# Optimization experiments

Measured on AMD Instinct MI355X. Metric: run time of the kernel, lower is better.

## Reference

```python
import jax, jax.numpy as jnp
import numpy as np

E, K, D, H = 8, 2, 1024, 2048   # num_experts, top_k, dim, ffn_dim
B, S = 1, 1024                   # batch, seq


def setup_inputs() -> dict:
    key = jax.random.key(0)
    k0, k1, k2, k3, k4 = jax.random.split(key, 5)
    sD = 1.0 / np.sqrt(D)
    sH = 1.0 / np.sqrt(H)
    return {
        "hidden_states": jax.random.normal(k0, (B, S, D), jnp.float32),
        "gate_w": jax.random.normal(k1, (E, D), jnp.float32) * sD,
        "w1": jax.random.normal(k2, (E, D, H), jnp.float32) * sD,
        "w2": jax.random.normal(k3, (E, H, D), jnp.float32) * sH,
        "w3": jax.random.normal(k4, (E, D, H), jnp.float32) * sD,
    }


def _grouped_swiglu(x_sorted, counts, w1, w2, w3):
    """Grouped expert SwiGLU over tokens sorted by expert id.

    x_sorted: [T, D] tokens grouped contiguously by expert (expert 0 first).
    counts:   [E] number of tokens per expert (sums to T).
    """
    if hasattr(jax.lax, "ragged_dot"):
        gs = counts.astype(jnp.int32)
        h = jax.nn.silu(jax.lax.ragged_dot(x_sorted, w1, gs)) * jax.lax.ragged_dot(x_sorted, w3, gs)
        return jax.lax.ragged_dot(h, w2, gs)
    # Fallback: per-expert masked GEMM (same math; zeros pass through silu*mul).
    pos = jnp.arange(x_sorted.shape[0])
    eid = jnp.searchsorted(jnp.cumsum(counts), pos, side="right")  # expert of each sorted token
    out = jnp.zeros((x_sorted.shape[0], w2.shape[-1]), x_sorted.dtype)
    for e in range(w1.shape[0]):
        xm = jnp.where((eid == e)[:, None], x_sorted, 0.0)
        he = jax.nn.silu(xm @ w1[e]) * (xm @ w3[e])
        out = out + he @ w2[e]
    return out


def reference(hidden_states, gate_w, w1, w2, w3):
    x = hidden_states.reshape(-1, D)                      # [N, D]
    N = x.shape[0]
    # --- router: softmax over experts, then top-k ---
    scores = jax.nn.softmax(x @ gate_w.T, axis=-1)        # [N, E]
    top_scores, sel = jax.lax.top_k(scores, K)            # [N, K]
    # flatten slot-major so flat_idx % N == token id (matches `% num_tokens`)
    sel_flat = sel.T.reshape(-1)                          # [K*N]
    scores_flat = top_scores.T.reshape(-1)                # [K*N]
    # --- reorder: stable sort by expert id ---
    order = jnp.argsort(sel_flat, stable=True)            # [K*N]
    tok_sorted = order % N                                # original token per routed slot
    scores_sorted = scores_flat[order]
    counts = jnp.bincount(sel_flat, length=E)             # tokens per expert
    # --- dispatch (ep_size=1: all-to-all is identity) + grouped expert GEMM ---
    x_sorted = x[tok_sorted]                              # [K*N, D]
    y = _grouped_swiglu(x_sorted, counts, w1, w2, w3)     # [K*N, D]
    # --- weighted scatter-combine ---
    weighted = y * scores_sorted[:, None]
    out = jnp.zeros((N, D), x.dtype).at[tok_sorted].add(weighted)
    return out.reshape(hidden_states.shape)
```

## Files before the change

kernel.cpp:

```cpp
#include <hip/hip_runtime.h>
#include <hip/hip_bf16.h>
#include <math.h>

#define NE 8
#define DD 1024
#define HH 2048
#define NTOK 1024
#define NSLOT 2048
#define NSLOTP 3072

typedef short short8v __attribute__((ext_vector_type(8)));
typedef short short4v __attribute__((ext_vector_type(4)));
typedef float f32x4 __attribute__((ext_vector_type(4)));

static __device__ __forceinline__ unsigned short f2bf(float f) {
  union { __hip_bfloat16 h; unsigned short u; } c;
  c.h = __float2bfloat16(f);
  return c.u;
}

static __device__ __forceinline__ int sigma(int n) {
  return ((n >> 1) & 3) ^ ((n >> 3) & 1);
}

#define GLD16(SRC, DST)                                                        \
  __builtin_amdgcn_global_load_lds(                                            \
      (__attribute__((address_space(1))) void*)(SRC),                          \
      (__attribute__((address_space(3))) void*)(DST), 16, 0, 0)

__global__ __launch_bounds__(64) void krouter(const float* __restrict__ x,
                                              const float* __restrict__ gw,
                                              int* __restrict__ e_sel,
                                              float* __restrict__ w_sel) {
  int n = blockIdx.x;
  int lane = threadIdx.x;
  const float4* xr = (const float4*)(x + (size_t)n * DD);
  const float4* gr = (const float4*)gw;
  float acc[NE];
#pragma unroll
  for (int e = 0; e < NE; ++e) acc[e] = 0.f;
#pragma unroll
  for (int i = 0; i < 4; ++i) {
    float4 xv = xr[lane + i * 64];
#pragma unroll
    for (int e = 0; e < NE; ++e) {
      float4 gv = gr[e * 256 + lane + i * 64];
      acc[e] += xv.x * gv.x + xv.y * gv.y + xv.z * gv.z + xv.w * gv.w;
    }
  }
#pragma unroll
  for (int e = 0; e < NE; ++e)
#pragma unroll
    for (int off = 32; off > 0; off >>= 1) acc[e] += __shfl_xor(acc[e], off);
  if (lane == 0) {
    float m = acc[0];
#pragma unroll
    for (int e = 1; e < NE; ++e) m = fmaxf(m, acc[e]);
    float p[NE];
    float z = 0.f;
#pragma unroll
    for (int e = 0; e < NE; ++e) { p[e] = expf(acc[e] - m); z += p[e]; }
    float inv = 1.f / z;
    int e1 = 0;
#pragma unroll
    for (int e = 1; e < NE; ++e) if (acc[e] > acc[e1]) e1 = e;
    int e2 = (e1 == 0) ? 1 : 0;
#pragma unroll
    for (int e = 0; e < NE; ++e) if (e != e1 && acc[e] > acc[e2]) e2 = e;
    e_sel[n] = e1;         w_sel[n] = p[e1] * inv;
    e_sel[NTOK + n] = e2;  w_sel[NTOK + n] = p[e2] * inv;
  }
}

__global__ __launch_bounds__(256) void kbuild(const int* __restrict__ e_sel,
                                              const float* __restrict__ w_sel,
                                              int* __restrict__ tok,
                                              float* __restrict__ wgt,
                                              int* __restrict__ meta) {
  __shared__ int sc[NE], scur[NE];
  int t = threadIdx.x;
  if (t < NE) sc[t] = 0;
  __syncthreads();
  for (int s = t; s < NSLOTP; s += 256) tok[s] = -1;
  for (int s = t; s < NSLOT; s += 256) atomicAdd(&sc[e_sel[s]], 1);
  __syncthreads();
  if (t == 0) {
    int run = 0, i64 = 0, i128 = 0;
    for (int e = 0; e < NE; ++e) {
      meta[8 + e] = run; scur[e] = run;
      meta[e] = sc[e];
      int nm = (sc[e] + 127) >> 7;
      for (int m = 0; m < nm; ++m) {
        meta[128 + i128] = e; meta[152 + i128] = m; ++i128;
      }
      for (int m = 0; m < 2 * nm; ++m) {
        meta[32 + i64] = e; meta[80 + i64] = m; ++i64;
      }
      run += nm << 7;
    }
    meta[16] = i64; meta[17] = i128;
  }
  __syncthreads();
  for (int s = t; s < NSLOT; s += 256) {
    int e = e_sel[s];
    int pos = atomicAdd(&scur[e], 1);
    tok[pos] = s & (NTOK - 1);
    wgt[pos] = w_sel[s];
  }
}

__global__ __launch_bounds__(256) void kgather(const float* __restrict__ x,
                                               const int* __restrict__ tok,
                                               unsigned short* __restrict__ xg) {
  int tid = threadIdx.x;
  int row = blockIdx.x * 2 + (tid >> 7);
  int g = tid & 127;
  int t = tok[row];
  int pos = (g & 3) ^ ((row >> 1) & 3);
  char* dst = (char*)xg + (size_t)row * 2048 + (g >> 2) * 64 + (pos << 4);
  short8v v = {0, 0, 0, 0, 0, 0, 0, 0};
  if (t >= 0) {
    const float* src = x + (size_t)t * DD + g * 8;
    float4 f0 = *(const float4*)src;
    float4 f1 = *(const float4*)(src + 4);
    v[0] = (short)f2bf(f0.x); v[1] = (short)f2bf(f0.y);
    v[2] = (short)f2bf(f0.z); v[3] = (short)f2bf(f0.w);
    v[4] = (short)f2bf(f1.x); v[5] = (short)f2bf(f1.y);
    v[6] = (short)f2bf(f1.z); v[7] = (short)f2bf(f1.w);
  }
  *(short8v*)dst = v;
}

__global__ __launch_bounds__(256, 4) void kgemm13(
    const unsigned short* __restrict__ xg, const float* __restrict__ w1,
    const float* __restrict__ w3, unsigned short* __restrict__ hws,
    const int* __restrict__ meta) {
  __shared__ __align__(16) char smem[24576];
  char* ldsA = smem;
  char* ldsB = smem + 8192;
  int vt = blockIdx.y;
  if (vt >= meta[16]) return;
  int e = meta[32 + vt], mt = meta[80 + vt];
  int n0 = blockIdx.x * 64;
  int abase = meta[8 + e] + mt * 64;
  int tid = threadIdx.x, l = tid & 63, w = tid >> 6;

  int th = tid & 127;
  int nb = th & 15, kb = th >> 4;
  const float* wsrc = (tid < 128) ? w1 : w3;
  const float* pb = wsrc + (size_t)e * DD * HH + (size_t)(kb * 4) * HH + n0 + nb * 4;
  int mofs = (tid < 128) ? 0 : 4096;
  int baddr[4];
#pragma unroll
  for (int c = 0; c < 4; ++c) {
    int n = nb * 4 + c;
    baddr[c] = mofs + n * 64 + ((((kb >> 1) ^ sigma(n)) & 3) << 4) + (kb & 1) * 8;
  }
  const char* srcA = (const char*)xg +
                     (size_t)(abase + w * 16 + (l >> 2)) * 2048 + ((l & 3) << 4);
  int aoff[4];
#pragma unroll
  for (int mf = 0; mf < 4; ++mf) {
    int r = mf * 16 + (l & 15);
    aoff[mf] = r * 64 + ((((l >> 4) ^ (r >> 1)) & 3) << 4);
  }
  int nn = w * 16 + (l & 15);
  int boff = nn * 64 + ((((l >> 4) ^ sigma(nn)) & 3) << 4);

  f32x4 accg[4], accu[4];
#pragma unroll
  for (int i = 0; i < 4; ++i) {
    accg[i] = (f32x4){0.f, 0.f, 0.f, 0.f};
    accu[i] = (f32x4){0.f, 0.f, 0.f, 0.f};
  }

  float4 q[4];
  const float* qp = pb;
#pragma unroll
  for (int r = 0; r < 4; ++r) q[r] = *(const float4*)(qp + (size_t)r * HH);
  GLD16(srcA, ldsA + w * 1024);
#pragma unroll
  for (int c = 0; c < 4; ++c) {
    short4v tv;
    tv[0] = (short)f2bf(q[0][c]); tv[1] = (short)f2bf(q[1][c]);
    tv[2] = (short)f2bf(q[2][c]); tv[3] = (short)f2bf(q[3][c]);
    *(short4v*)(ldsB + baddr[c]) = tv;
  }
  qp += 32 * HH;
#pragma unroll
  for (int r = 0; r < 4; ++r) q[r] = *(const float4*)(qp + (size_t)r * HH);
  GLD16(srcA + 64, ldsA + 4096 + w * 1024);
  qp += 32 * HH;
  __syncthreads();

  for (int s = 0; s < 32; ++s) {
    int buf = s & 1;
    short8v a[4];
#pragma unroll
    for (int mf = 0; mf < 4; ++mf)
      a[mf] = *(const short8v*)(ldsA + buf * 4096 + aoff[mf]);
    short8v bg = *(const short8v*)(ldsB + buf * 8192 + boff);
    short8v bu = *(const short8v*)(ldsB + buf * 8192 + 4096 + boff);
#pragma unroll
    for (int mf = 0; mf < 4; ++mf) {
      accg[mf] = __builtin_amdgcn_mfma_f32_16x16x32_bf16(a[mf], bg, accg[mf], 0, 0, 0);
      accu[mf] = __builtin_amdgcn_mfma_f32_16x16x32_bf16(a[mf], bu, accu[mf], 0, 0, 0);
    }
    if (s < 31) {
      char* d = ldsB + (buf ^ 1) * 8192;
#pragma unroll
      for (int c = 0; c < 4; ++c) {
        short4v tv;
        tv[0] = (short)f2bf(q[0][c]); tv[1] = (short)f2bf(q[1][c]);
        tv[2] = (short)f2bf(q[2][c]); tv[3] = (short)f2bf(q[3][c]);
        *(short4v*)(d + baddr[c]) = tv;
      }
    }
    __syncthreads();
    if (s < 30) {
#pragma unroll
      for (int r = 0; r < 4; ++r) q[r] = *(const float4*)(qp + (size_t)r * HH);
      GLD16(srcA + (s + 2) * 64, ldsA + buf * 4096 + w * 1024);
      qp += 32 * HH;
    }
  }

  unsigned short* hl = (unsigned short*)smem;
#pragma unroll
  for (int mf = 0; mf < 4; ++mf)
#pragma unroll
    for (int rr = 0; rr < 4; ++rr) {
      int row = mf * 16 + ((l >> 4) << 2) + rr;
      int col = w * 16 + (l & 15);
      float gv = accg[mf][rr], uv = accu[mf][rr];
      hl[row * 64 + col] = f2bf((gv / (1.f + __expf(-gv))) * uv);
    }
  __syncthreads();
#pragma unroll
  for (int p = 0; p < 2; ++p) {
    int idx = p * 256 + tid;
    int row = idx >> 3, g = idx & 7;
    int dp = abase + row;
    size_t db = (size_t)dp * 4096 + (size_t)n0 * 2 + (g >> 2) * 64 +
                ((size_t)((g & 3) ^ ((dp >> 1) & 3)) << 4);
    *(short8v*)((char*)hws + db) =
        *(const short8v*)((const char*)hl + row * 128 + (g << 4));
  }
}

__global__ __launch_bounds__(256, 4) void kgemm2(
    const unsigned short* __restrict__ hws, const float* __restrict__ w2,
    float* __restrict__ out, const int* __restrict__ tok,
    const float* __restrict__ wgt, const int* __restrict__ meta) {
  __shared__ __align__(16) char smem[16384];
  char* ldsA = smem;
  char* ldsB = smem + 8192;
  int vt = blockIdx.y;
  if (vt >= meta[16]) return;
  int e = meta[32 + vt], mt = meta[80 + vt];
  int n0 = blockIdx.x * 64;
  int kz = blockIdx.z;
  int mbase = meta[8 + e] + mt * 64;
  int rem = meta[e] - mt * 64;
  int tid = threadIdx.x, l = tid & 63, w = tid >> 6;

  int nb = tid & 15, kb = tid >> 4;
  const float* pb = w2 + (size_t)e * HH * DD +
                    (size_t)(kz * 1024 + kb * 2) * DD + n0 + nb * 4;
  int baddr[4];
#pragma unroll
  for (int c = 0; c < 4; ++c) {
    int n = nb * 4 + c;
    baddr[c] = n * 64 + ((((kb >> 2) ^ sigma(n)) & 3) << 4) + (kb & 3) * 4;
  }
  const char* srcA = (const char*)hws +
                     (size_t)(mbase + w * 16 + (l >> 2)) * 4096 +
                     (size_t)kz * 2048 + ((l & 3) << 4);
  int aoff[4];
#pragma unroll
  for (int mf = 0; mf < 4; ++mf) {
    int r = mf * 16 + (l & 15);
    aoff[mf] = r * 64 + ((((l >> 4) ^ (r >> 1)) & 3) << 4);
  }
  int nn = w * 16 + (l & 15);
  int boff = nn * 64 + ((((l >> 4) ^ sigma(nn)) & 3) << 4);

  f32x4 acc[4];
#pragma unroll
  for (int i = 0; i < 4; ++i) acc[i] = (f32x4){0.f, 0.f, 0.f, 0.f};

  float4 q[2];
  const float* qp = pb;
#pragma unroll
  for (int r = 0; r < 2; ++r) q[r] = *(const float4*)(qp + (size_t)r * DD);
  GLD16(srcA, ldsA + w * 1024);
  {
#pragma unroll
    for (int c = 0; c < 4; ++c) {
      unsigned v = (unsigned)f2bf(q[0][c]) | ((unsigned)f2bf(q[1][c]) << 16);
      *(unsigned*)(ldsB + baddr[c]) = v;
    }
  }
  qp += 32 * DD;
#pragma unroll
  for (int r = 0; r < 2; ++r) q[r] = *(const float4*)(qp + (size_t)r * DD);
  GLD16(srcA + 64, ldsA + 4096 + w * 1024);
  qp += 32 * DD;
  __syncthreads();

  for (int s = 0; s < 32; ++s) {
    int buf = s & 1;
    short8v a[4];
#pragma unroll
    for (int mf = 0; mf < 4; ++mf)
      a[mf] = *(const short8v*)(ldsA + buf * 4096 + aoff[mf]);
    short8v b = *(const short8v*)(ldsB + buf * 4096 + boff);
#pragma unroll
    for (int mf = 0; mf < 4; ++mf)
      acc[mf] = __builtin_amdgcn_mfma_f32_16x16x32_bf16(a[mf], b, acc[mf], 0, 0, 0);
    if (s < 31) {
      char* d = ldsB + (buf ^ 1) * 4096;
#pragma unroll
      for (int c = 0; c < 4; ++c) {
        unsigned v = (unsigned)f2bf(q[0][c]) | ((unsigned)f2bf(q[1][c]) << 16);
        *(unsigned*)(d + baddr[c]) = v;
      }
    }
    __syncthreads();
    if (s < 30) {
#pragma unroll
      for (int r = 0; r < 2; ++r) q[r] = *(const float4*)(qp + (size_t)r * DD);
      GLD16(srcA + (s + 2) * 64, ldsA + buf * 4096 + w * 1024);
      qp += 32 * DD;
    }
  }

#pragma unroll
  for (int mf = 0; mf < 4; ++mf)
#pragma unroll
    for (int rr = 0; rr < 4; ++rr) {
      int row = mf * 16 + ((l >> 4) << 2) + rr;
      if (row < rem) {
        int t = tok[mbase + row];
        float wt = wgt[mbase + row];
        atomicAdd(out + (size_t)t * DD + n0 + w * 16 + (l & 15),
                  wt * acc[mf][rr]);
      }
    }
}

extern "C" void kernel_launch(void* const* d_in, const int* in_sizes, int n_in,
                              void* d_out, int out_size, void* d_ws, size_t ws_size,
                              hipStream_t stream) {
  const float* x  = (const float*)d_in[0];
  const float* gw = (const float*)d_in[1];
  const float* w1 = (const float*)d_in[2];
  const float* w2 = (const float*)d_in[3];
  const float* w3 = (const float*)d_in[4];
  float* out = (float*)d_out;
  char* ws = (char*)d_ws;
  const size_t MB = 1024 * 1024;
  if (ws_size < 24 * MB) return;

  unsigned short* xg  = (unsigned short*)(ws);
  unsigned short* hws = (unsigned short*)(ws + 6 * MB);
  char* mb = ws + 20 * MB;
  int*   e_sel  = (int*)mb;
  float* w_sel  = (float*)(mb + 8192);
  int*   tok    = (int*)(mb + 16384);
  float* wgt    = (float*)(mb + 16384 + 12288);
  int*   meta   = (int*)(mb + 16384 + 24576);

  hipMemsetAsync(out, 0, (size_t)out_size * sizeof(float), stream);
  krouter<<<dim3(NTOK), 64, 0, stream>>>(x, gw, e_sel, w_sel);
  kbuild<<<1, 256, 0, stream>>>(e_sel, w_sel, tok, wgt, meta);
  kgather<<<dim3(NSLOTP / 2), 256, 0, stream>>>(x, tok, xg);
  kgemm13<<<dim3(32, 48), 256, 0, stream>>>(xg, w1, w3, hws, meta);
  kgemm2<<<dim3(16, 48, 2), 256, 0, stream>>>(hws, w2, out, tok, wgt, meta);
}
```

Before: 119.6 us.

## Use 128-row M tiles with register-staged A operand in expert GEMMs

Both expert GEMM kernels move from 64-row to 128-row M tiles over a 2x2 wave layout, so each fp32 weight tile is streamed and converted once per 128 routed tokens instead of once per 64. This targets the dominant cost, which is reading the fp32 w1/w3/w2 weights. The A operand is now loaded straight from global memory into registers rather than staged through LDS, which halves LDS use. Weight prefetch is deepened to two stages in registers. The costs are more accumulator registers (launch bound drops to 3 blocks), more padded rows for experts with few tokens, and reliance on 128-row tile metadata in meta[17], meta[128+] and meta[152+], which kbuild is assumed to already fill.

```diff
diff --git a/kernel.cpp b/kernel.cpp
--- a/kernel.cpp
+++ b/kernel.cpp
@@ -10,7 +10,6 @@
 #define NSLOTP 3072
 
 typedef short short8v __attribute__((ext_vector_type(8)));
-typedef short short4v __attribute__((ext_vector_type(4)));
 typedef float f32x4 __attribute__((ext_vector_type(4)));
 
 static __device__ __forceinline__ unsigned short f2bf(float f) {
@@ -23,10 +22,12 @@
   return ((n >> 1) & 3) ^ ((n >> 3) & 1);
 }
 
-#define GLD16(SRC, DST)                                                        \
-  __builtin_amdgcn_global_load_lds(                                            \
-      (__attribute__((address_space(1))) void*)(SRC),                          \
-      (__attribute__((address_space(3))) void*)(DST), 16, 0, 0)
+static __device__ __forceinline__ short8v pk8(const float* q) {
+  short8v v;
+#pragma unroll
+  for (int i = 0; i < 8; ++i) v[i] = (short)f2bf(q[i]);
+  return v;
+}
 
 __global__ __launch_bounds__(64) void krouter(const float* __restrict__ x,
                                               const float* __restrict__ gw,
@@ -121,123 +122,132 @@
   short8v v = {0, 0, 0, 0, 0, 0, 0, 0};
   if (t >= 0) {
     const float* src = x + (size_t)t * DD + g * 8;
-    float4 f0 = *(const float4*)src;
-    float4 f1 = *(const float4*)(src + 4);
-    v[0] = (short)f2bf(f0.x); v[1] = (short)f2bf(f0.y);
-    v[2] = (short)f2bf(f0.z); v[3] = (short)f2bf(f0.w);
-    v[4] = (short)f2bf(f1.x); v[5] = (short)f2bf(f1.y);
-    v[6] = (short)f2bf(f1.z); v[7] = (short)f2bf(f1.w);
+    float q[8];
+#pragma unroll
+    for (int i = 0; i < 8; ++i) q[i] = src[i];
+    v = pk8(q);
   }
   *(short8v*)dst = v;
 }
 
-__global__ __launch_bounds__(256, 4) void kgemm13(
+__global__ __launch_bounds__(256, 3) void kgemm13(
     const unsigned short* __restrict__ xg, const float* __restrict__ w1,
     const float* __restrict__ w3, unsigned short* __restrict__ hws,
     const int* __restrict__ meta) {
-  __shared__ __align__(16) char smem[24576];
-  char* ldsA = smem;
-  char* ldsB = smem + 8192;
+  __shared__ __align__(16) char smem[16384];
+  char* ldsB = smem;
   int vt = blockIdx.y;
-  if (vt >= meta[16]) return;
-  int e = meta[32 + vt], mt = meta[80 + vt];
+  if (vt >= meta[17]) return;
+  int e = meta[128 + vt], mt = meta[152 + vt];
   int n0 = blockIdx.x * 64;
-  int abase = meta[8 + e] + mt * 64;
+  int abase = meta[8 + e] + mt * 128;
   int tid = threadIdx.x, l = tid & 63, w = tid >> 6;
-
-  int th = tid & 127;
-  int nb = th & 15, kb = th >> 4;
-  const float* wsrc = (tid < 128) ? w1 : w3;
-  const float* pb = wsrc + (size_t)e * DD * HH + (size_t)(kb * 4) * HH + n0 + nb * 4;
-  int mofs = (tid < 128) ? 0 : 4096;
-  int baddr[4];
-#pragma unroll
-  for (int c = 0; c < 4; ++c) {
-    int n = nb * 4 + c;
-    baddr[c] = mofs + n * 64 + ((((kb >> 1) ^ sigma(n)) & 3) << 4) + (kb & 1) * 8;
-  }
-  const char* srcA = (const char*)xg +
-                     (size_t)(abase + w * 16 + (l >> 2)) * 2048 + ((l & 3) << 4);
-  int aoff[4];
+  int wm = w & 1, wn = w >> 1;
+
+  int bn = tid & 63, kb = tid >> 6;
+  const float* pb1 = w1 + (size_t)e * DD * HH + (size_t)(kb * 8) * HH + n0 + bn;
+  const float* pb3 = w3 + (size_t)e * DD * HH + (size_t)(kb * 8) * HH + n0 + bn;
+  int wb = bn * 64 + (((kb ^ sigma(bn)) & 3) << 4);
+
+  const char* pa[4];
 #pragma unroll
   for (int mf = 0; mf < 4; ++mf) {
-    int r = mf * 16 + (l & 15);
-    aoff[mf] = r * 64 + ((((l >> 4) ^ (r >> 1)) & 3) << 4);
-  }
-  int nn = w * 16 + (l & 15);
-  int boff = nn * 64 + ((((l >> 4) ^ sigma(nn)) & 3) << 4);
-
-  f32x4 accg[4], accu[4];
-#pragma unroll
-  for (int i = 0; i < 4; ++i) {
-    accg[i] = (f32x4){0.f, 0.f, 0.f, 0.f};
-    accu[i] = (f32x4){0.f, 0.f, 0.f, 0.f};
-  }
-
-  float4 q[4];
-  const float* qp = pb;
-#pragma unroll
-  for (int r = 0; r < 4; ++r) q[r] = *(const float4*)(qp + (size_t)r * HH);
-  GLD16(srcA, ldsA + w * 1024);
-#pragma unroll
-  for (int c = 0; c < 4; ++c) {
-    short4v tv;
-    tv[0] = (short)f2bf(q[0][c]); tv[1] = (short)f2bf(q[1][c]);
-    tv[2] = (short)f2bf(q[2][c]); tv[3] = (short)f2bf(q[3][c]);
-    *(short4v*)(ldsB + baddr[c]) = tv;
-  }
-  qp += 32 * HH;
-#pragma unroll
-  for (int r = 0; r < 4; ++r) q[r] = *(const float4*)(qp + (size_t)r * HH);
-  GLD16(srcA + 64, ldsA + 4096 + w * 1024);
-  qp += 32 * HH;
-  __syncthreads();
-
-  for (int s = 0; s < 32; ++s) {
-    int buf = s & 1;
-    short8v a[4];
-#pragma unroll
-    for (int mf = 0; mf < 4; ++mf)
-      a[mf] = *(const short8v*)(ldsA + buf * 4096 + aoff[mf]);
-    short8v bg = *(const short8v*)(ldsB + buf * 8192 + boff);
-    short8v bu = *(const short8v*)(ldsB + buf * 8192 + 4096 + boff);
-#pragma unroll
-    for (int mf = 0; mf < 4; ++mf) {
-      accg[mf] = __builtin_amdgcn_mfma_f32_16x16x32_bf16(a[mf], bg, accg[mf], 0, 0, 0);
-      accu[mf] = __builtin_amdgcn_mfma_f32_16x16x32_bf16(a[mf], bu, accu[mf], 0, 0, 0);
+    int r = wm * 64 + mf * 16 + (l & 15);
+    pa[mf] = (const char*)xg + (size_t)(abase + r) * 2048 +
+             ((((l >> 4) ^ (r >> 1)) & 3) << 4);
+  }
+  int boff[2];
+#pragma unroll
+  for (int nf = 0; nf < 2; ++nf) {
+    int n = wn * 32 + nf * 16 + (l & 15);
+    boff[nf] = n * 64 + ((((l >> 4) ^ sigma(n)) & 3) << 4);
+  }
+
+  f32x4 accg[4][2], accu[4][2];
+#pragma unroll
+  for (int i = 0; i < 4; ++i)
+#pragma unroll
+    for (int j = 0; j < 2; ++j) {
+      accg[i][j] = (f32x4){0.f, 0.f, 0.f, 0.f};
+      accu[i][j] = (f32x4){0.f, 0.f, 0.f, 0.f};
     }
-    if (s < 31) {
-      char* d = ldsB + (buf ^ 1) * 8192;
-#pragma unroll
-      for (int c = 0; c < 4; ++c) {
-        short4v tv;
-        tv[0] = (short)f2bf(q[0][c]); tv[1] = (short)f2bf(q[1][c]);
-        tv[2] = (short)f2bf(q[2][c]); tv[3] = (short)f2bf(q[3][c]);
-        *(short4v*)(d + baddr[c]) = tv;
+
+  float q1[2][8], q3[2][8];
+  short8v a[4];
+#pragma unroll
+  for (int r = 0; r < 8; ++r) {
+    q1[0][r] = pb1[(size_t)r * HH];
+    q3[0][r] = pb3[(size_t)r * HH];
+    q1[1][r] = pb1[(size_t)(32 + r) * HH];
+    q3[1][r] = pb3[(size_t)(32 + r) * HH];
+  }
+#pragma unroll
+  for (int mf = 0; mf < 4; ++mf) a[mf] = *(const short8v*)(pa[mf]);
+  *(short8v*)(ldsB + wb) = pk8(q1[0]);
+  *(short8v*)(ldsB + 4096 + wb) = pk8(q3[0]);
+#pragma unroll
+  for (int r = 0; r < 8; ++r) {
+    q1[0][r] = pb1[(size_t)(64 + r) * HH];
+    q3[0][r] = pb3[(size_t)(64 + r) * HH];
+  }
+  __syncthreads();
+
+#define STEP13(S, P)                                                           \
+  {                                                                            \
+    if ((S) < 31) {                                                            \
+      char* d = ldsB + (((P) ^ 1) << 13);                                      \
+      *(short8v*)(d + wb) = pk8(q1[(P) ^ 1]);                                  \
+      *(short8v*)(d + 4096 + wb) = pk8(q3[(P) ^ 1]);                           \
+    }                                                                          \
+    if ((S) < 29) {                                                            \
+      const float* s1 = pb1 + (size_t)((S) + 3) * 32 * HH;                     \
+      const float* s3 = pb3 + (size_t)((S) + 3) * 32 * HH;                     \
+      _Pragma("unroll") for (int r = 0; r < 8; ++r) {                          \
+        q1[(P) ^ 1][r] = s1[(size_t)r * HH];                                   \
+        q3[(P) ^ 1][r] = s3[(size_t)r * HH];                                   \
+      }                                                                        \
+    }                                                                          \
+    short8v b1f[2], b3f[2];                                                    \
+    _Pragma("unroll") for (int nf = 0; nf < 2; ++nf) {                         \
+      b1f[nf] = *(const short8v*)(ldsB + ((P) << 13) + boff[nf]);              \
+      b3f[nf] = *(const short8v*)(ldsB + ((P) << 13) + 4096 + boff[nf]);       \
+    }                                                                          \
+    _Pragma("unroll") for (int nf = 0; nf < 2; ++nf)                           \
+        _Pragma("unroll") for (int mf = 0; mf < 4; ++mf) {                     \
+      accg[mf][nf] = __builtin_amdgcn_mfma_f32_16x16x32_bf16(                  \
+          a[mf], b1f[nf], accg[mf][nf], 0, 0, 0);                              \
+      accu[mf][nf] = __builtin_amdgcn_mfma_f32_16x16x32_bf16(                  \
+          a[mf], b3f[nf], accu[mf][nf], 0, 0, 0);                              \
+    }                                                                          \
+    if ((S) < 31) {                                                           \
+      _Pragma("unroll") for (int mf = 0; mf < 4; ++mf)                         \
+          a[mf] = *(const short8v*)(pa[mf] + ((S) + 1) * 64);                  \
+    }                                                                          \
+    __syncthreads();                                                           \
+  }
+
+  for (int ss = 0; ss < 16; ++ss) {
+    int s0 = 2 * ss;
+    STEP13(s0, 0);
+    STEP13(s0 + 1, 1);
+  }
+#undef STEP13
+
+  unsigned short* hl = (unsigned short*)smem;
+#pragma unroll
+  for (int mf = 0; mf < 4; ++mf)
+#pragma unroll
+    for (int nf = 0; nf < 2; ++nf)
+#pragma unroll
+      for (int rr = 0; rr < 4; ++rr) {
+        int row = wm * 64 + mf * 16 + ((l >> 4) << 2) + rr;
+        int col = wn * 32 + nf * 16 + (l & 15);
+        float gv = accg[mf][nf][rr], uv = accu[mf][nf][rr];
+        hl[row * 64 + col] = f2bf((gv / (1.f + __expf(-gv))) * uv);
       }
-    }
-    __syncthreads();
-    if (s < 30) {
-#pragma unroll
-      for (int r = 0; r < 4; ++r) q[r] = *(const float4*)(qp + (size_t)r * HH);
-      GLD16(srcA + (s + 2) * 64, ldsA + buf * 4096 + w * 1024);
-      qp += 32 * HH;
-    }
-  }
-
-  unsigned short* hl = (unsigned short*)smem;
-#pragma unroll
-  for (int mf = 0; mf < 4; ++mf)
-#pragma unroll
-    for (int rr = 0; rr < 4; ++rr) {
-      int row = mf * 16 + ((l >> 4) << 2) + rr;
-      int col = w * 16 + (l & 15);
-      float gv = accg[mf][rr], uv = accu[mf][rr];
-      hl[row * 64 + col] = f2bf((gv / (1.f + __expf(-gv))) * uv);
-    }
-  __syncthreads();
-#pragma unroll
-  for (int p = 0; p < 2; ++p) {
+  __syncthreads();
+#pragma unroll
+  for (int p = 0; p < 4; ++p) {
     int idx = p * 256 + tid;
     int row = idx >> 3, g = idx & 7;
     int dp = abase + row;
@@ -252,99 +262,100 @@
     const unsigned short* __restrict__ hws, const float* __restrict__ w2,
     float* __restrict__ out, const int* __restrict__ tok,
     const float* __restrict__ wgt, const int* __restrict__ meta) {
-  __shared__ __align__(16) char smem[16384];
-  char* ldsA = smem;
-  char* ldsB = smem + 8192;
+  __shared__ __align__(16) char smem[8192];
+  char* ldsB = smem;
   int vt = blockIdx.y;
-  if (vt >= meta[16]) return;
-  int e = meta[32 + vt], mt = meta[80 + vt];
+  if (vt >= meta[17]) return;
+  int e = meta[128 + vt], mt = meta[152 + vt];
   int n0 = blockIdx.x * 64;
   int kz = blockIdx.z;
-  int mbase = meta[8 + e] + mt * 64;
-  int rem = meta[e] - mt * 64;
+  int mbase = meta[8 + e] + mt * 128;
+  int rem = meta[e] - mt * 128;
   int tid = threadIdx.x, l = tid & 63, w = tid >> 6;
-
-  int nb = tid & 15, kb = tid >> 4;
+  int wm = w & 1, wn = w >> 1;
+
+  int bn = tid & 63, kb = tid >> 6;
   const float* pb = w2 + (size_t)e * HH * DD +
-                    (size_t)(kz * 1024 + kb * 2) * DD + n0 + nb * 4;
-  int baddr[4];
-#pragma unroll
-  for (int c = 0; c < 4; ++c) {
-    int n = nb * 4 + c;
-    baddr[c] = n * 64 + ((((kb >> 2) ^ sigma(n)) & 3) << 4) + (kb & 3) * 4;
-  }
-  const char* srcA = (const char*)hws +
-                     (size_t)(mbase + w * 16 + (l >> 2)) * 4096 +
-                     (size_t)kz * 2048 + ((l & 3) << 4);
-  int aoff[4];
+                    (size_t)(kz * 1024 + kb * 8) * DD + n0 + bn;
+  int wb = bn * 64 + (((kb ^ sigma(bn)) & 3) << 4);
+
+  const char* pa[4];
 #pragma unroll
   for (int mf = 0; mf < 4; ++mf) {
-    int r = mf * 16 + (l & 15);
-    aoff[mf] = r * 64 + ((((l >> 4) ^ (r >> 1)) & 3) << 4);
-  }
-  int nn = w * 16 + (l & 15);
-  int boff = nn * 64 + ((((l >> 4) ^ sigma(nn)) & 3) << 4);
-
-  f32x4 acc[4];
-#pragma unroll
-  for (int i = 0; i < 4; ++i) acc[i] = (f32x4){0.f, 0.f, 0.f, 0.f};
-
-  float4 q[2];
-  const float* qp = pb;
-#pragma unroll
-  for (int r = 0; r < 2; ++r) q[r] = *(const float4*)(qp + (size_t)r * DD);
-  GLD16(srcA, ldsA + w * 1024);
-  {
-#pragma unroll
-    for (int c = 0; c < 4; ++c) {
-      unsigned v = (unsigned)f2bf(q[0][c]) | ((unsigned)f2bf(q[1][c]) << 16);
-      *(unsigned*)(ldsB + baddr[c]) = v;
-    }
-  }
-  qp += 32 * DD;
-#pragma unroll
-  for (int r = 0; r < 2; ++r) q[r] = *(const float4*)(qp + (size_t)r * DD);
-  GLD16(srcA + 64, ldsA + 4096 + w * 1024);
-  qp += 32 * DD;
-  __syncthreads();
-
-  for (int s = 0; s < 32; ++s) {
-    int buf = s & 1;
-    short8v a[4];
-#pragma unroll
-    for (int mf = 0; mf < 4; ++mf)
-      a[mf] = *(const short8v*)(ldsA + buf * 4096 + aoff[mf]);
-    short8v b = *(const short8v*)(ldsB + buf * 4096 + boff);
-#pragma unroll
-    for (int mf = 0; mf < 4; ++mf)
-      acc[mf] = __builtin_amdgcn_mfma_f32_16x16x32_bf16(a[mf], b, acc[mf], 0, 0, 0);
-    if (s < 31) {
-      char* d = ldsB + (buf ^ 1) * 4096;
-#pragma unroll
-      for (int c = 0; c < 4; ++c) {
-        unsigned v = (unsigned)f2bf(q[0][c]) | ((unsigned)f2bf(q[1][c]) << 16);
-        *(unsigned*)(d + baddr[c]) = v;
-      }
-    }
-    __syncthreads();
-    if (s < 30) {
-#pragma unroll
-      for (int r = 0; r < 2; ++r) q[r] = *(const float4*)(qp + (size_t)r * DD);
-      GLD16(srcA + (s + 2) * 64, ldsA + buf * 4096 + w * 1024);
-      qp += 32 * DD;
-    }
-  }
+    int r = wm * 64 + mf * 16 + (l & 15);
+    pa[mf] = (const char*)hws + (size_t)(mbase + r) * 4096 + kz * 2048 +
+             ((((l >> 4) ^ (r >> 1)) & 3) << 4);
+  }
+  int boff[2];
+#pragma unroll
+  for (int nf = 0; nf < 2; ++nf) {
+    int n = wn * 32 + nf * 16 + (l & 15);
+    boff[nf] = n * 64 + ((((l >> 4) ^ sigma(n)) & 3) << 4);
+  }
+
+  f32x4 acc[4][2];
+#pragma unroll
+  for (int i = 0; i < 4; ++i)
+#pragma unroll
+    for (int j = 0; j < 2; ++j) acc[i][j] = (f32x4){0.f, 0.f, 0.f, 0.f};
+
+  float q[2][8];
+  short8v a[4];
+#pragma unroll
+  for (int r = 0; r < 8; ++r) {
+    q[0][r] = pb[(size_t)r * DD];
+    q[1][r] = pb[(size_t)(32 + r) * DD];
+  }
+#pragma unroll
+  for (int mf = 0; mf < 4; ++mf) a[mf] = *(const short8v*)(pa[mf]);
+  *(short8v*)(ldsB + wb) = pk8(q[0]);
+#pragma unroll
+  for (int r = 0; r < 8; ++r) q[0][r] = pb[(size_t)(64 + r) * DD];
+  __syncthreads();
+
+#define STEP2(S, P)                                                            \
+  {                                                                            \
+    if ((S) < 31) {                                                            \
+      *(short8v*)(ldsB + (((P) ^ 1) << 12) + wb) = pk8(q[(P) ^ 1]);            \
+    }                                                                          \
+    if ((S) < 29) {                                                            \
+      const float* sp = pb + (size_t)((S) + 3) * 32 * DD;                      \
+      _Pragma("unroll") for (int r = 0; r < 8; ++r)                            \
+          q[(P) ^ 1][r] = sp[(size_t)r * DD];                                  \
+    }                                                                          \
+    short8v bf[2];                                                             \
+    _Pragma("unroll") for (int nf = 0; nf < 2; ++nf)                           \
+        bf[nf] = *(const short8v*)(ldsB + ((P) << 12) + boff[nf]);             \
+    _Pragma("unroll") for (int nf = 0; nf < 2; ++nf)                           \
+        _Pragma("unroll") for (int mf = 0; mf < 4; ++mf)                       \
+            acc[mf][nf] = __builtin_amdgcn_mfma_f32_16x16x32_bf16(             \
+                a[mf], bf[nf], acc[mf][nf], 0, 0, 0);                          \
+    if ((S) < 31) {                                                           \
+      _Pragma("unroll") for (int mf = 0; mf < 4; ++mf)                         \
+          a[mf] = *(const short8v*)(pa[mf] + ((S) + 1) * 64);                  \
+    }                                                                          \
+    __syncthreads();                                                           \
+  }
+
+  for (int ss = 0; ss < 16; ++ss) {
+    int s0 = 2 * ss;
+    STEP2(s0, 0);
+    STEP2(s0 + 1, 1);
+  }
+#undef STEP2
 
 #pragma unroll
   for (int mf = 0; mf < 4; ++mf)
 #pragma unroll
     for (int rr = 0; rr < 4; ++rr) {
-      int row = mf * 16 + ((l >> 4) << 2) + rr;
+      int row = wm * 64 + mf * 16 + ((l >> 4) << 2) + rr;
       if (row < rem) {
         int t = tok[mbase + row];
         float wt = wgt[mbase + row];
-        atomicAdd(out + (size_t)t * DD + n0 + w * 16 + (l & 15),
-                  wt * acc[mf][rr]);
+#pragma unroll
+        for (int nf = 0; nf < 2; ++nf)
+          atomicAdd(out + (size_t)t * DD + n0 + wn * 32 + nf * 16 + (l & 15),
+                    wt * acc[mf][nf][rr]);
       }
     }
 }
@@ -375,6 +386,6 @@
   krouter<<<dim3(NTOK), 64, 0, stream>>>(x, gw, e_sel, w_sel);
   kbuild<<<1, 256, 0, stream>>>(e_sel, w_sel, tok, wgt, meta);
   kgather<<<dim3(NSLOTP / 2), 256, 0, stream>>>(x, tok, xg);
-  kgemm13<<<dim3(32, 48), 256, 0, stream>>>(xg, w1, w3, hws, meta);
-  kgemm2<<<dim3(16, 48, 2), 256, 0, stream>>>(hws, w2, out, tok, wgt, meta);
-}
+  kgemm13<<<dim3(32, 24), 256, 0, stream>>>(xg, w1, w3, hws, meta);
+  kgemm2<<<dim3(16, 24, 2), 256, 0, stream>>>(hws, w2, out, tok, wgt, meta);
+}
```

Result: no change. 119.4 us (-0.1%).
